# Kernel optimization log

Hardware: AMD Instinct MI355X
Metric: run time of the kernel (lower is better)

The kernel has to match this reference:

```python
import jax, jax.numpy as jnp
import numpy as np

B, T, C = 8, 2048, 1024
HS, HO = 64, 64  # head_size, head_output_dim

def setup_inputs() -> dict:
    key = jax.random.key(0)
    k1, k2, k3, k4 = jax.random.split(key, 4)
    x = jax.random.normal(k1, (B, T, C), dtype=jnp.float32)
    Wk = jax.random.normal(k2, (HS, C), dtype=jnp.float32) * (C ** -0.5)
    Wq = jax.random.normal(k3, (HS, C), dtype=jnp.float32) * (C ** -0.5)
    Wv = jax.random.normal(k4, (HO, C), dtype=jnp.float32) * (C ** -0.5)
    return {"x": x, "Wk": Wk, "Wq": Wq, "Wv": Wv}

def reference(x, Wk, Wq, Wv):
    Bx, Tx, Cx = x.shape
    k = jnp.einsum('btc,hc->bth', x, Wk)  # [B,T,HS]
    q = jnp.einsum('btc,hc->bth', x, Wq)  # [B,T,HS]
    v = jnp.einsum('btc,oc->bto', x, Wv)  # [B,T,HO]
    scores = jnp.einsum('bth,bsh->bts', q, k)  # [B,T,T]
    causal = jnp.tril(jnp.ones((Tx, Tx), dtype=bool))
    scores = jnp.where(causal, scores, -jnp.inf)
    # original scales AFTER masking; -inf * scale stays -inf, same softmax result
    weights = jax.nn.softmax(scores * (HS ** -0.5), axis=-1)
    return jnp.einsum('bts,bso->bto', weights, v)
```

## Files before the change

kernel.cpp:

```cpp
#include <hip/hip_runtime.h>
#include <hip/hip_bf16.h>

typedef __attribute__((ext_vector_type(8))) short short8;
typedef __attribute__((ext_vector_type(4))) float float4v;

#define LOG2E 1.44269504088896340736f

__device__ __forceinline__ unsigned short f2bf(float f) {
    unsigned int u = __float_as_uint(f);
    unsigned int r = (u + 0x7fffu + ((u >> 16) & 1u)) >> 16;
    return (unsigned short)r;
}

__device__ __forceinline__ float4v ntload4(const float* p) {
    return __builtin_nontemporal_load((const float4v*)p);
}

__global__ void wconv_kernel(const float* __restrict__ Wk, const float* __restrict__ Wq,
                             const float* __restrict__ Wv, unsigned short* __restrict__ Wb) {
    int i = blockIdx.x * 256 + threadIdx.x;
    if (i >= 192 * 1024) return;
    float v;
    if (i < 65536)       v = Wk[i];
    else if (i < 131072) v = Wq[i - 65536];
    else                 v = Wv[i - 131072];
    Wb[i] = f2bf(v);
}

__global__ __launch_bounds__(256) void proj_kernel(
    const float* __restrict__ x, const unsigned short* __restrict__ Wb,
    unsigned short* __restrict__ qs, unsigned short* __restrict__ ks,
    unsigned short* __restrict__ vT) {
    __shared__ unsigned short Bl[2][192 * 72];

    const int tid  = threadIdx.x;
    const int lane = tid & 63;
    const int wave = tid >> 6;
    const int rg   = wave & 1;
    const int g    = wave >> 1;
    const int quad = lane >> 4;
    const int l16  = lane & 15;
    const int t0   = blockIdx.x * 32;

    const int srow = tid >> 3;
    const int scol = (tid & 7) * 8;

    const int rowA = t0 + rg * 16 + l16;
    const float* xr = x + (size_t)rowA * 1024;

    float4v acc[6];
#pragma unroll
    for (int n = 0; n < 6; n++) acc[n] = (float4v){0.f, 0.f, 0.f, 0.f};

    short8 breg[6];
#pragma unroll
    for (int i = 0; i < 6; i++)
        breg[i] = *(const short8*)(Wb + (size_t)(i * 32 + srow) * 1024 + scol);
    float4v areg[4];
    areg[0] = ntload4(xr + quad * 8);
    areg[1] = ntload4(xr + quad * 8 + 4);
    areg[2] = ntload4(xr + 32 + quad * 8);
    areg[3] = ntload4(xr + 32 + quad * 8 + 4);
#pragma unroll
    for (int i = 0; i < 6; i++)
        *(short8*)&Bl[0][(i * 32 + srow) * 72 + scol] = breg[i];
    __syncthreads();

#pragma unroll 2
    for (int kt = 0; kt < 16; kt++) {
        const int kn = ((kt + 1) & 15) * 64;
        short8 bnext[6];
#pragma unroll
        for (int i = 0; i < 6; i++)
            bnext[i] = *(const short8*)(Wb + (size_t)(i * 32 + srow) * 1024 + kn + scol);
        float4v anext[4];
        anext[0] = ntload4(xr + kn + quad * 8);
        anext[1] = ntload4(xr + kn + quad * 8 + 4);
        anext[2] = ntload4(xr + kn + 32 + quad * 8);
        anext[3] = ntload4(xr + kn + 32 + quad * 8 + 4);
        const unsigned short* Bc = Bl[kt & 1];
#pragma unroll
        for (int kc = 0; kc < 2; kc++) {
            short8 af;
#pragma unroll
            for (int j = 0; j < 4; j++) af[j] = (short)f2bf(areg[kc * 2][j]);
#pragma unroll
            for (int j = 0; j < 4; j++) af[4 + j] = (short)f2bf(areg[kc * 2 + 1][j]);
#pragma unroll
            for (int n = 0; n < 6; n++) {
                const short8 bf = *(const short8*)&Bc[((g * 6 + n) * 16 + l16) * 72 + kc * 32 + quad * 8];
                acc[n] = __builtin_amdgcn_mfma_f32_16x16x32_bf16(af, bf, acc[n], 0, 0, 0);
            }
        }
        unsigned short* Bn = (unsigned short*)Bl[(kt + 1) & 1];
#pragma unroll
        for (int i = 0; i < 6; i++)
            *(short8*)&Bn[(i * 32 + srow) * 72 + scol] = bnext[i];
        __syncthreads();
#pragma unroll
        for (int i = 0; i < 4; i++) areg[i] = anext[i];
    }

    const int rowD = t0 + rg * 16 + quad * 4;
#pragma unroll
    for (int r = 0; r < 4; r++) {
        const int t = rowD + r;
        const int b = t >> 11, tt = t & 2047;
        if (g == 0) {
#pragma unroll
            for (int n = 0; n < 4; n++)
                ks[(size_t)t * 64 + n * 16 + l16] = f2bf(acc[n][r]);
#pragma unroll
            for (int n = 4; n < 6; n++)
                qs[(size_t)t * 64 + (n - 4) * 16 + l16] = f2bf(acc[n][r] * 0.125f);
        } else {
#pragma unroll
            for (int n = 0; n < 2; n++)
                qs[(size_t)t * 64 + (n + 2) * 16 + l16] = f2bf(acc[n][r] * 0.125f);
#pragma unroll
            for (int n = 2; n < 6; n++)
                vT[(size_t)b * 131072 + (size_t)((n - 2) * 16 + l16) * 2048 + tt] = f2bf(acc[n][r]);
        }
    }
}

__global__ __launch_bounds__(128) void attn_kernel(
    const unsigned short* __restrict__ qs, const unsigned short* __restrict__ ks,
    const unsigned short* __restrict__ vT, float* __restrict__ out) {
    __shared__ unsigned short Kl[2][64 * 72];
    __shared__ unsigned short Vl[2][64 * 72];
    __shared__ unsigned short P[2][16 * 72];

    const int tid  = threadIdx.x;
    const int lane = tid & 63;
    const int wave = tid >> 6;
    const int quad = lane >> 4;
    const int l16  = lane & 15;
    const int bx   = blockIdx.x;
    const int h    = bx >> 8;
    const int m    = bx & 255;
    const int b    = m & 7;
    const int jj   = m >> 3;
    const int qt2  = h ? (63 - jj) : jj;
    const int t0   = qt2 * 32;

    const unsigned short* qb = qs + (size_t)b * 131072;
    const unsigned short* kb = ks + (size_t)b * 131072;
    const unsigned short* vb = vT + (size_t)b * 131072;

    const int srow = tid >> 3;
    const int scol = (tid & 7) * 8;

    const int qrow = t0 + wave * 16 + l16;
    const short8 qf0 = *(const short8*)(qb + (size_t)qrow * 64 + quad * 8);
    const short8 qf1 = *(const short8*)(qb + (size_t)qrow * 64 + 32 + quad * 8);

    float4v o[4];
#pragma unroll
    for (int ot = 0; ot < 4; ot++) o[ot] = (float4v){0.f, 0.f, 0.f, 0.f};
    float lrow = 0.f;

    const int nkb = qt2 / 2 + 1;

#pragma unroll
    for (int i2 = 0; i2 < 4; i2++) {
        short8 kv = *(const short8*)(kb + (size_t)(i2 * 16 + srow) * 64 + scol);
        short8 vv = *(const short8*)(vb + (size_t)(i2 * 16 + srow) * 2048 + scol);
        *(short8*)&Kl[0][(i2 * 16 + srow) * 72 + scol] = kv;
        *(short8*)&Vl[0][(i2 * 16 + srow) * 72 + scol] = vv;
    }
    __syncthreads();

    for (int j = 0; j < nkb; j++) {
        const int buf = j & 1;
        const int key0n = (j + 1 < nkb ? j + 1 : j) * 64;
        short8 kn[4], vn[4];
#pragma unroll
        for (int i2 = 0; i2 < 4; i2++) {
            kn[i2] = *(const short8*)(kb + (size_t)(key0n + i2 * 16 + srow) * 64 + scol);
            vn[i2] = *(const short8*)(vb + (size_t)(i2 * 16 + srow) * 2048 + key0n + scol);
        }

        float4v s[4];
#pragma unroll
        for (int kt = 0; kt < 4; kt++) {
            const short8 ka = *(const short8*)&Kl[buf][(kt * 16 + l16) * 72 + quad * 8];
            const short8 kc = *(const short8*)&Kl[buf][(kt * 16 + l16) * 72 + 32 + quad * 8];
            float4v z = (float4v){0.f, 0.f, 0.f, 0.f};
            z = __builtin_amdgcn_mfma_f32_16x16x32_bf16(ka, qf0, z, 0, 0, 0);
            s[kt] = __builtin_amdgcn_mfma_f32_16x16x32_bf16(kc, qf1, z, 0, 0, 0);
        }
        if (j == nkb - 1) {
#pragma unroll
            for (int kt = 0; kt < 4; kt++)
#pragma unroll
                for (int r = 0; r < 4; r++)
                    if (j * 64 + kt * 16 + quad * 4 + r > qrow) s[kt][r] = -1e30f;
        }
#pragma unroll
        for (int kt = 0; kt < 4; kt++) {
            float p0 = exp2f(s[kt][0] * LOG2E);
            float p1 = exp2f(s[kt][1] * LOG2E);
            float p2 = exp2f(s[kt][2] * LOG2E);
            float p3 = exp2f(s[kt][3] * LOG2E);
            lrow += (p0 + p1) + (p2 + p3);
            unsigned int lo = (unsigned int)f2bf(p0) | ((unsigned int)f2bf(p1) << 16);
            unsigned int hi = (unsigned int)f2bf(p2) | ((unsigned int)f2bf(p3) << 16);
            unsigned long long w = ((unsigned long long)hi << 32) | lo;
            *(unsigned long long*)&P[wave][l16 * 72 + kt * 16 + quad * 4] = w;
        }
#pragma unroll
        for (int kc = 0; kc < 2; kc++) {
            const short8 pf = *(const short8*)&P[wave][l16 * 72 + kc * 32 + quad * 8];
#pragma unroll
            for (int ot = 0; ot < 4; ot++) {
                const short8 vf = *(const short8*)&Vl[buf][(ot * 16 + l16) * 72 + kc * 32 + quad * 8];
                o[ot] = __builtin_amdgcn_mfma_f32_16x16x32_bf16(pf, vf, o[ot], 0, 0, 0);
            }
        }
#pragma unroll
        for (int i2 = 0; i2 < 4; i2++) {
            *(short8*)&Kl[buf ^ 1][(i2 * 16 + srow) * 72 + scol] = kn[i2];
            *(short8*)&Vl[buf ^ 1][(i2 * 16 + srow) * 72 + scol] = vn[i2];
        }
        __syncthreads();
    }

    lrow += __shfl_xor(lrow, 16);
    lrow += __shfl_xor(lrow, 32);
#pragma unroll
    for (int r = 0; r < 4; r++) {
        const float inv = 1.0f / __shfl(lrow, quad * 4 + r);
        const int t = t0 + wave * 16 + quad * 4 + r;
        float* ob = out + (size_t)b * 131072 + (size_t)t * 64;
#pragma unroll
        for (int ot = 0; ot < 4; ot++) ob[ot * 16 + l16] = o[ot][r] * inv;
    }
}

extern "C" void kernel_launch(void* const* d_in, const int* in_sizes, int n_in,
                              void* d_out, int out_size, void* d_ws, size_t ws_size,
                              hipStream_t stream) {
    const float* x  = (const float*)d_in[0];
    const float* Wk = (const float*)d_in[1];
    const float* Wq = (const float*)d_in[2];
    const float* Wv = (const float*)d_in[3];
    float* out = (float*)d_out;

    unsigned short* Wb  = (unsigned short*)d_ws;
    unsigned short* qsb = (unsigned short*)((char*)d_ws + 393216);
    unsigned short* ksb = qsb + 1048576;
    unsigned short* vTb = ksb + 1048576;

    hipLaunchKernelGGL(wconv_kernel, dim3(768), dim3(256), 0, stream, Wk, Wq, Wv, Wb);
    hipLaunchKernelGGL(proj_kernel, dim3(512), dim3(256), 0, stream, x, Wb, qsb, ksb, vTb);
    hipLaunchKernelGGL(attn_kernel, dim3(512), dim3(128), 0, stream, qsb, ksb, vTb, out);
}
```

Baseline: 159.7 us.

## Split attention keys across waves with cross-wave reduction; use regular x loads

Restructures the attention kernel so each block handles 16 query rows, and its four waves each process a different 64-key tile within a 256-key super-block. Partial outputs and row sums are reduced through shared memory at the end. The grid doubles to 1024 blocks of 256 threads. The aim is more parallelism per query tile and shorter serial key loops. The trade-off is the lost double-buffered prefetch, an extra reduction pass and larger LDS use. The projection kernel also swaps nontemporal x loads for ordinary loads.

```diff
diff --git a/kernel.cpp b/kernel.cpp
--- a/kernel.cpp
+++ b/kernel.cpp
@@ -10,10 +10,6 @@
     unsigned int u = __float_as_uint(f);
     unsigned int r = (u + 0x7fffu + ((u >> 16) & 1u)) >> 16;
     return (unsigned short)r;
-}
-
-__device__ __forceinline__ float4v ntload4(const float* p) {
-    return __builtin_nontemporal_load((const float4v*)p);
 }
 
 __global__ void wconv_kernel(const float* __restrict__ Wk, const float* __restrict__ Wq,
@@ -57,10 +53,10 @@
     for (int i = 0; i < 6; i++)
         breg[i] = *(const short8*)(Wb + (size_t)(i * 32 + srow) * 1024 + scol);
     float4v areg[4];
-    areg[0] = ntload4(xr + quad * 8);
-    areg[1] = ntload4(xr + quad * 8 + 4);
-    areg[2] = ntload4(xr + 32 + quad * 8);
-    areg[3] = ntload4(xr + 32 + quad * 8 + 4);
+    areg[0] = *(const float4v*)(xr + quad * 8);
+    areg[1] = *(const float4v*)(xr + quad * 8 + 4);
+    areg[2] = *(const float4v*)(xr + 32 + quad * 8);
+    areg[3] = *(const float4v*)(xr + 32 + quad * 8 + 4);
 #pragma unroll
     for (int i = 0; i < 6; i++)
         *(short8*)&Bl[0][(i * 32 + srow) * 72 + scol] = breg[i];
@@ -74,10 +70,10 @@
         for (int i = 0; i < 6; i++)
             bnext[i] = *(const short8*)(Wb + (size_t)(i * 32 + srow) * 1024 + kn + scol);
         float4v anext[4];
-        anext[0] = ntload4(xr + kn + quad * 8);
-        anext[1] = ntload4(xr + kn + quad * 8 + 4);
-        anext[2] = ntload4(xr + kn + 32 + quad * 8);
-        anext[3] = ntload4(xr + kn + 32 + quad * 8 + 4);
+        anext[0] = *(const float4v*)(xr + kn + quad * 8);
+        anext[1] = *(const float4v*)(xr + kn + quad * 8 + 4);
+        anext[2] = *(const float4v*)(xr + kn + 32 + quad * 8);
+        anext[3] = *(const float4v*)(xr + kn + 32 + quad * 8 + 4);
         const unsigned short* Bc = Bl[kt & 1];
 #pragma unroll
         for (int kc = 0; kc < 2; kc++) {
@@ -124,12 +120,14 @@
     }
 }
 
-__global__ __launch_bounds__(128) void attn_kernel(
+__global__ __launch_bounds__(256) void attn_kernel(
     const unsigned short* __restrict__ qs, const unsigned short* __restrict__ ks,
     const unsigned short* __restrict__ vT, float* __restrict__ out) {
-    __shared__ unsigned short Kl[2][64 * 72];
-    __shared__ unsigned short Vl[2][64 * 72];
-    __shared__ unsigned short P[2][16 * 72];
+    __shared__ unsigned short Kl[4 * 64 * 72];
+    __shared__ unsigned short Vl[64 * 264];
+    __shared__ unsigned short P[4][16 * 72];
+    __shared__ float Ll[4][16];
+    float* Of = (float*)Kl;
 
     const int tid  = threadIdx.x;
     const int lane = tid & 63;
@@ -137,104 +135,117 @@
     const int quad = lane >> 4;
     const int l16  = lane & 15;
     const int bx   = blockIdx.x;
-    const int h    = bx >> 8;
-    const int m    = bx & 255;
-    const int b    = m & 7;
-    const int jj   = m >> 3;
-    const int qt2  = h ? (63 - jj) : jj;
-    const int t0   = qt2 * 32;
+    const int b    = bx & 7;
+    const int i    = bx >> 3;
+    const int qt   = (i & 1) ? (127 - (i >> 1)) : (i >> 1);
+    const int t0   = qt * 16;
 
     const unsigned short* qb = qs + (size_t)b * 131072;
     const unsigned short* kb = ks + (size_t)b * 131072;
     const unsigned short* vb = vT + (size_t)b * 131072;
 
-    const int srow = tid >> 3;
-    const int scol = (tid & 7) * 8;
-
-    const int qrow = t0 + wave * 16 + l16;
+    const int ksr = tid >> 3;
+    const int ksc = (tid & 7) * 8;
+    const int vsr = tid >> 5;
+    const int vsc = (tid & 31) * 8;
+
+    const int qrow = t0 + l16;
     const short8 qf0 = *(const short8*)(qb + (size_t)qrow * 64 + quad * 8);
     const short8 qf1 = *(const short8*)(qb + (size_t)qrow * 64 + 32 + quad * 8);
 
     float4v o[4];
 #pragma unroll
     for (int ot = 0; ot < 4; ot++) o[ot] = (float4v){0.f, 0.f, 0.f, 0.f};
-    float lrow = 0.f;
-
-    const int nkb = qt2 / 2 + 1;
-
-#pragma unroll
-    for (int i2 = 0; i2 < 4; i2++) {
-        short8 kv = *(const short8*)(kb + (size_t)(i2 * 16 + srow) * 64 + scol);
-        short8 vv = *(const short8*)(vb + (size_t)(i2 * 16 + srow) * 2048 + scol);
-        *(short8*)&Kl[0][(i2 * 16 + srow) * 72 + scol] = kv;
-        *(short8*)&Vl[0][(i2 * 16 + srow) * 72 + scol] = vv;
-    }
+    float lpart = 0.f;
+
+    const int nkb  = (qt >> 2) + 1;
+    const int nsup = (nkb + 3) >> 2;
+
+    for (int s = 0; s < nsup; s++) {
+        const int key0 = s * 256;
+        __syncthreads();
+#pragma unroll
+        for (int i2 = 0; i2 < 8; i2++) {
+            int kr = key0 + i2 * 32 + ksr; kr = kr < 2047 ? kr : 2047;
+            *(short8*)&Kl[(i2 * 32 + ksr) * 72 + ksc] = *(const short8*)(kb + (size_t)kr * 64 + ksc);
+        }
+#pragma unroll
+        for (int i2 = 0; i2 < 8; i2++) {
+            const int orow = i2 * 8 + vsr;
+            int kc2 = key0 + vsc; kc2 = kc2 < 2040 ? kc2 : 2040;
+            *(short8*)&Vl[orow * 264 + vsc] = *(const short8*)(vb + (size_t)orow * 2048 + kc2);
+        }
+        __syncthreads();
+
+        const int jt = s * 4 + wave;
+        if (jt < nkb) {
+            const int kbase = wave * 64;
+            float4v sv[4];
+#pragma unroll
+            for (int kt = 0; kt < 4; kt++) {
+                const short8 ka = *(const short8*)&Kl[(kbase + kt * 16 + l16) * 72 + quad * 8];
+                const short8 kc = *(const short8*)&Kl[(kbase + kt * 16 + l16) * 72 + 32 + quad * 8];
+                float4v z = (float4v){0.f, 0.f, 0.f, 0.f};
+                z = __builtin_amdgcn_mfma_f32_16x16x32_bf16(ka, qf0, z, 0, 0, 0);
+                sv[kt] = __builtin_amdgcn_mfma_f32_16x16x32_bf16(kc, qf1, z, 0, 0, 0);
+            }
+            if (jt == nkb - 1) {
+#pragma unroll
+                for (int kt = 0; kt < 4; kt++)
+#pragma unroll
+                    for (int r = 0; r < 4; r++)
+                        if (jt * 64 + kt * 16 + quad * 4 + r > qrow) sv[kt][r] = -1e30f;
+            }
+#pragma unroll
+            for (int kt = 0; kt < 4; kt++) {
+                float p0 = exp2f(sv[kt][0] * LOG2E);
+                float p1 = exp2f(sv[kt][1] * LOG2E);
+                float p2 = exp2f(sv[kt][2] * LOG2E);
+                float p3 = exp2f(sv[kt][3] * LOG2E);
+                lpart += (p0 + p1) + (p2 + p3);
+                unsigned int lo = (unsigned int)f2bf(p0) | ((unsigned int)f2bf(p1) << 16);
+                unsigned int hi = (unsigned int)f2bf(p2) | ((unsigned int)f2bf(p3) << 16);
+                unsigned long long w = ((unsigned long long)hi << 32) | lo;
+                *(unsigned long long*)&P[wave][l16 * 72 + kt * 16 + quad * 4] = w;
+            }
+#pragma unroll
+            for (int kc = 0; kc < 2; kc++) {
+                const short8 pf = *(const short8*)&P[wave][l16 * 72 + kc * 32 + quad * 8];
+#pragma unroll
+                for (int ot = 0; ot < 4; ot++) {
+                    const short8 vf = *(const short8*)&Vl[(ot * 16 + l16) * 264 + wave * 64 + kc * 32 + quad * 8];
+                    o[ot] = __builtin_amdgcn_mfma_f32_16x16x32_bf16(pf, vf, o[ot], 0, 0, 0);
+                }
+            }
+        }
+    }
+
+    lpart += __shfl_xor(lpart, 16);
+    lpart += __shfl_xor(lpart, 32);
     __syncthreads();
-
-    for (int j = 0; j < nkb; j++) {
-        const int buf = j & 1;
-        const int key0n = (j + 1 < nkb ? j + 1 : j) * 64;
-        short8 kn[4], vn[4];
-#pragma unroll
-        for (int i2 = 0; i2 < 4; i2++) {
-            kn[i2] = *(const short8*)(kb + (size_t)(key0n + i2 * 16 + srow) * 64 + scol);
-            vn[i2] = *(const short8*)(vb + (size_t)(i2 * 16 + srow) * 2048 + key0n + scol);
-        }
-
-        float4v s[4];
-#pragma unroll
-        for (int kt = 0; kt < 4; kt++) {
-            const short8 ka = *(const short8*)&Kl[buf][(kt * 16 + l16) * 72 + quad * 8];
-            const short8 kc = *(const short8*)&Kl[buf][(kt * 16 + l16) * 72 + 32 + quad * 8];
-            float4v z = (float4v){0.f, 0.f, 0.f, 0.f};
-            z = __builtin_amdgcn_mfma_f32_16x16x32_bf16(ka, qf0, z, 0, 0, 0);
-            s[kt] = __builtin_amdgcn_mfma_f32_16x16x32_bf16(kc, qf1, z, 0, 0, 0);
-        }
-        if (j == nkb - 1) {
-#pragma unroll
-            for (int kt = 0; kt < 4; kt++)
-#pragma unroll
-                for (int r = 0; r < 4; r++)
-                    if (j * 64 + kt * 16 + quad * 4 + r > qrow) s[kt][r] = -1e30f;
-        }
-#pragma unroll
-        for (int kt = 0; kt < 4; kt++) {
-            float p0 = exp2f(s[kt][0] * LOG2E);
-            float p1 = exp2f(s[kt][1] * LOG2E);
-            float p2 = exp2f(s[kt][2] * LOG2E);
-            float p3 = exp2f(s[kt][3] * LOG2E);
-            lrow += (p0 + p1) + (p2 + p3);
-            unsigned int lo = (unsigned int)f2bf(p0) | ((unsigned int)f2bf(p1) << 16);
-            unsigned int hi = (unsigned int)f2bf(p2) | ((unsigned int)f2bf(p3) << 16);
-            unsigned long long w = ((unsigned long long)hi << 32) | lo;
-            *(unsigned long long*)&P[wave][l16 * 72 + kt * 16 + quad * 4] = w;
-        }
-#pragma unroll
-        for (int kc = 0; kc < 2; kc++) {
-            const short8 pf = *(const short8*)&P[wave][l16 * 72 + kc * 32 + quad * 8];
-#pragma unroll
-            for (int ot = 0; ot < 4; ot++) {
-                const short8 vf = *(const short8*)&Vl[buf][(ot * 16 + l16) * 72 + kc * 32 + quad * 8];
-                o[ot] = __builtin_amdgcn_mfma_f32_16x16x32_bf16(pf, vf, o[ot], 0, 0, 0);
-            }
-        }
-#pragma unroll
-        for (int i2 = 0; i2 < 4; i2++) {
-            *(short8*)&Kl[buf ^ 1][(i2 * 16 + srow) * 72 + scol] = kn[i2];
-            *(short8*)&Vl[buf ^ 1][(i2 * 16 + srow) * 72 + scol] = vn[i2];
-        }
-        __syncthreads();
-    }
-
-    lrow += __shfl_xor(lrow, 16);
-    lrow += __shfl_xor(lrow, 32);
-#pragma unroll
-    for (int r = 0; r < 4; r++) {
-        const float inv = 1.0f / __shfl(lrow, quad * 4 + r);
-        const int t = t0 + wave * 16 + quad * 4 + r;
-        float* ob = out + (size_t)b * 131072 + (size_t)t * 64;
-#pragma unroll
-        for (int ot = 0; ot < 4; ot++) ob[ot * 16 + l16] = o[ot][r] * inv;
+#pragma unroll
+    for (int r = 0; r < 4; r++)
+#pragma unroll
+        for (int ot = 0; ot < 4; ot++)
+            Of[wave * 1088 + (quad * 4 + r) * 68 + ot * 16 + l16] = o[ot][r];
+    if (lane < 16) Ll[wave][lane] = lpart;
+    __syncthreads();
+
+    {
+        const int row = tid >> 4;
+        const int c0  = (tid & 15) * 4;
+        const float lsum = Ll[0][row] + Ll[1][row] + Ll[2][row] + Ll[3][row];
+        float4v v0 = *(const float4v*)&Of[0 * 1088 + row * 68 + c0];
+        float4v v1 = *(const float4v*)&Of[1 * 1088 + row * 68 + c0];
+        float4v v2 = *(const float4v*)&Of[2 * 1088 + row * 68 + c0];
+        float4v v3 = *(const float4v*)&Of[3 * 1088 + row * 68 + c0];
+        float4v res;
+        const float inv = 1.0f / lsum;
+#pragma unroll
+        for (int j = 0; j < 4; j++)
+            res[j] = ((v0[j] + v1[j]) + (v2[j] + v3[j])) * inv;
+        float* ob = out + (size_t)b * 131072 + (size_t)(t0 + row) * 64 + c0;
+        *(float4v*)ob = res;
     }
 }
 
@@ -254,5 +265,5 @@
 
     hipLaunchKernelGGL(wconv_kernel, dim3(768), dim3(256), 0, stream, Wk, Wq, Wv, Wb);
     hipLaunchKernelGGL(proj_kernel, dim3(512), dim3(256), 0, stream, x, Wb, qsb, ksb, vTb);
-    hipLaunchKernelGGL(attn_kernel, dim3(512), dim3(128), 0, stream, qsb, ksb, vTb, out);
-}
+    hipLaunchKernelGGL(attn_kernel, dim3(1024), dim3(256), 0, stream, qsb, ksb, vTb, out);
+}
```

Measured after the change: 152.4 us. 1.05x faster.
